# Kernel optimization log

Measured on AMD Instinct MI355X. Metric: run time of the kernel, lower is better.

Reference implementation:

```python
import jax, jax.numpy as jnp
import numpy as np

N, C, D_EMB = 4096, 8192, 512
SCALE = 3.0
KL_WEIGHT = 0.2


def _l2norm(x):
    # matches torch F.normalize(p=2, dim=-1) with eps clamp
    return x / jnp.maximum(jnp.linalg.norm(x, axis=-1, keepdims=True), 1e-12)


def setup_inputs() -> dict:
    key = jax.random.key(0)
    k1, k2, k3, k4 = jax.random.split(key, 4)
    X = jax.random.normal(k1, (N, D_EMB), dtype=jnp.float32)
    indices = jax.random.randint(k2, (N,), 0, N)
    T = jax.random.randint(k3, (N,), 0, C)
    proxies = jax.random.normal(k4, (C, D_EMB), dtype=jnp.float32) / 8.0
    sigmas_inv = jnp.full((C, D_EMB), np.log(np.e - 1.0), dtype=jnp.float32)
    return {"X": X, "indices": indices, "T": T, "proxies": proxies, "sigmas_inv": sigmas_inv}


def reference(X, indices, T, proxies, sigmas_inv):
    # per-class diagonal inverse-covariance weights s[c, d] = softplus(sigmas_inv)^2
    s = jax.nn.softplus(sigmas_inv) ** 2                        # (C, D)
    P = SCALE * _l2norm(proxies)                                # (C, D)
    Xn = SCALE * _l2norm(X)                                     # (N, D)
    # Mahalanobis-style distance D[n,c] = sum_d (x_nd - p_cd)^2 * s_cd
    Dmat = (Xn * Xn) @ s.T - 2.0 * (Xn @ (P * s).T) + jnp.sum(P * P * s, axis=-1)[None, :]  # (N, C)
    # log(softmax(-D)) == log_softmax(-D); one-hot targets (smoothing_const=0)
    logp = jax.nn.log_softmax(-Dmat, axis=-1)                   # (N, C)
    ce = -jnp.mean(logp[jnp.arange(Dmat.shape[0]), T])
    # KL regularizer: Sigma = 1/s, mu = normalized proxies
    Sig = 1.0 / s
    mus2 = _l2norm(proxies) ** 2
    kl = jnp.mean(jnp.sum(0.5 * (Sig + mus2 - 1.0 - jnp.log(Sig)), axis=-1))
    return ce + KL_WEIGHT * kl
```

## Files before the change

kernel.cpp:

```cpp
#include <hip/hip_runtime.h>
#include <hip/hip_bf16.h>
#include <cstdint>

#define N_ROWS 4096
#define N_CLS  8192
#define D_EMB  512
#define K_DIM  1024

using f32x4 = __attribute__((ext_vector_type(4))) float;

__device__ __forceinline__ float softplus_f(float v) {
  return (v > 20.f) ? v : log1pf(expf(v));
}

__device__ __forceinline__ unsigned short pack2_e4m3(float a, float b) {
  return (unsigned short)(__builtin_amdgcn_cvt_pk_fp8_f32(a, b, 0, false) & 0xffff);
}

__device__ __forceinline__ float e4m3_to_f(unsigned char v) {
  int e = (v >> 3) & 15, m = v & 7;
  float f;
  if (e) f = __uint_as_float((unsigned int)((e + 120) << 23) | ((unsigned int)m << 20));
  else   f = (float)m * 0.001953125f;
  return (v & 0x80) ? -f : f;
}

__device__ __forceinline__ float block_sum256(float v) {
  __shared__ float red[4];
  #pragma unroll
  for (int o = 32; o; o >>= 1) v += __shfl_xor(v, o);
  __syncthreads();
  if ((threadIdx.x & 63) == 0) red[threadIdx.x >> 6] = v;
  __syncthreads();
  return red[0] + red[1] + red[2] + red[3];
}

__device__ __forceinline__ void global_to_lds16(const void* g, void* l) {
  const __attribute__((address_space(1))) unsigned int* gp =
      reinterpret_cast<const __attribute__((address_space(1))) unsigned int*>(
          reinterpret_cast<uintptr_t>(g));
  __attribute__((address_space(3))) unsigned int* lp =
      reinterpret_cast<__attribute__((address_space(3))) unsigned int*>(
          reinterpret_cast<uintptr_t>(l));
  __builtin_amdgcn_global_load_lds(gp, lp, 16, 0, 0);
}

__global__ __launch_bounds__(256) void k_prep(const float* __restrict__ proxies,
                                              const float* __restrict__ sigmas_inv,
                                              const float* __restrict__ X,
                                              unsigned char* __restrict__ Bmat,
                                              unsigned char* __restrict__ Amat,
                                              float* __restrict__ tvec,
                                              float* __restrict__ klc) {
  const int bid = blockIdx.x;
  const int tid = threadIdx.x;
  if (bid < N_CLS) {
    const int c = bid;
    const float* p  = proxies    + (size_t)c * D_EMB;
    const float* si = sigmas_inv + (size_t)c * D_EMB;
    float2 p2 = ((const float2*)p)[tid];
    float ss = block_sum256(p2.x * p2.x + p2.y * p2.y);
    float invn = 1.0f / fmaxf(sqrtf(ss), 1e-12f);
    float2 s2 = ((const float2*)si)[tid];
    float sp0 = softplus_f(s2.x), sp1 = softplus_f(s2.y);
    float s0 = sp0 * sp0, s1 = sp1 * sp1;
    float pn0 = p2.x * invn, pn1 = p2.y * invn;
    float P0 = 3.0f * pn0, P1 = 3.0f * pn1;
    unsigned short* brow = (unsigned short*)(Bmat + (size_t)c * K_DIM);
    brow[tid]       = pack2_e4m3(s0, s1);
    brow[256 + tid] = pack2_e4m3(P0 * s0, P1 * s1);
    float tc = P0 * P0 * s0 + P1 * P1 * s1;
    float kl = 0.5f * (1.0f / s0 + pn0 * pn0 - 1.0f + 2.0f * logf(sp0))
             + 0.5f * (1.0f / s1 + pn1 * pn1 - 1.0f + 2.0f * logf(sp1));
    tc = block_sum256(tc);
    kl = block_sum256(kl);
    if (tid == 0) { tvec[c] = tc; klc[c] = kl; }
  } else {
    const int n = bid - N_CLS;
    const float* x = X + (size_t)n * D_EMB;
    float2 x2 = ((const float2*)x)[tid];
    float ss = block_sum256(x2.x * x2.x + x2.y * x2.y);
    float invn = 3.0f / fmaxf(sqrtf(ss), 1e-12f);
    float v0 = x2.x * invn, v1 = x2.y * invn;
    unsigned short* arow = (unsigned short*)(Amat + (size_t)n * K_DIM);
    arow[tid]       = pack2_e4m3(-v0 * v0, -v1 * v1);
    arow[256 + tid] = pack2_e4m3(2.0f * v0, 2.0f * v1);
  }
}

__global__ __launch_bounds__(256, 5) void k_gemm_lse(const unsigned char* __restrict__ Amat,
                                                     const unsigned char* __restrict__ Bmat,
                                                     const float* __restrict__ tvec,
                                                     float* __restrict__ Pm,
                                                     float* __restrict__ Psum) {
  __shared__ __align__(16) unsigned char lds[32768];
  const int tid  = threadIdx.x;
  const int lane = tid & 63;
  const int wave = tid >> 6;
  const int wr = wave >> 1, wc = wave & 1;
  const int swz  = ((int)blockIdx.x & 7) * 256 + ((int)blockIdx.x >> 3);
  const int rt   = swz & 31;
  const int ct   = swz >> 5;
  const int row0 = rt * 128;
  const int col0 = ct * 128;

  f32x4 acc[4][4];
  #pragma unroll
  for (int i = 0; i < 4; ++i)
    #pragma unroll
    for (int j = 0; j < 4; ++j) acc[i][j] = (f32x4){0.f, 0.f, 0.f, 0.f};

  const int arow = wr * 64 + (lane & 15);
  const int bcol = wc * 64 + (lane & 15);
  const int kb8  = (lane >> 4) * 8;

  const int f0  = tid * 16;
  const int f1  = 4096 + tid * 16;
  const int sf0 = f0 ^ (((f0 >> 7) & 7) << 4);
  const int sf1 = f1 ^ (((f1 >> 7) & 7) << 4);
  const unsigned char* gA0 = Amat + (size_t)(row0 + (sf0 >> 6)) * K_DIM + (sf0 & 63);
  const unsigned char* gA1 = Amat + (size_t)(row0 + (sf1 >> 6)) * K_DIM + (sf1 & 63);
  const unsigned char* gB0 = Bmat + (size_t)(col0 + (sf0 >> 6)) * K_DIM + (sf0 & 63);
  const unsigned char* gB1 = Bmat + (size_t)(col0 + (sf1 >> 6)) * K_DIM + (sf1 & 63);

  auto stg = [&](int slot, int ko) {
    unsigned char* la = lds + slot * 8192;
    unsigned char* lb = lds + 16384 + slot * 8192;
    global_to_lds16(gA0 + ko, la + f0);
    global_to_lds16(gA1 + ko, la + f1);
    global_to_lds16(gB0 + ko, lb + f0);
    global_to_lds16(gB1 + ko, lb + f1);
  };
  auto ld64 = [&](const unsigned char* base, int row, int kb) -> long {
    int f = row * 64 + kb;
    return *(const long*)(base + (f ^ (((f >> 7) & 7) << 4)));
  };

  stg(0, 0);
  __syncthreads();
  for (int t = 0; t < 16; ++t) {
    if (t < 15) stg((t + 1) & 1, (t + 1) * 64);
    const unsigned char* Ab = lds + (t & 1) * 8192;
    const unsigned char* Bb = lds + 16384 + (t & 1) * 8192;
    __builtin_amdgcn_s_setprio(1);
    #pragma unroll
    for (int ks = 0; ks < 64; ks += 32) {
      long a[4], b[4];
      #pragma unroll
      for (int mi = 0; mi < 4; ++mi) a[mi] = ld64(Ab, arow + mi * 16, ks + kb8);
      #pragma unroll
      for (int ni = 0; ni < 4; ++ni) b[ni] = ld64(Bb, bcol + ni * 16, ks + kb8);
      #pragma unroll
      for (int mi = 0; mi < 4; ++mi)
        #pragma unroll
        for (int ni = 0; ni < 4; ++ni)
          acc[mi][ni] = __builtin_amdgcn_mfma_f32_16x16x32_fp8_fp8(a[mi], b[ni], acc[mi][ni], 0, 0, 0);
    }
    __builtin_amdgcn_s_setprio(0);
    __syncthreads();
  }

  float (*ms)[2][2] = (float (*)[2][2])lds;
  float tc[4];
  #pragma unroll
  for (int ni = 0; ni < 4; ++ni)
    tc[ni] = tvec[col0 + wc * 64 + ni * 16 + (lane & 15)];

  #pragma unroll
  for (int mi = 0; mi < 4; ++mi) {
    #pragma unroll
    for (int j = 0; j < 4; ++j) {
      float z0 = acc[mi][0][j] - tc[0];
      float z1 = acc[mi][1][j] - tc[1];
      float z2 = acc[mi][2][j] - tc[2];
      float z3 = acc[mi][3][j] - tc[3];
      float m = fmaxf(fmaxf(z0, z1), fmaxf(z2, z3));
      #pragma unroll
      for (int o = 1; o < 16; o <<= 1) m = fmaxf(m, __shfl_xor(m, o));
      float s = __expf(z0 - m) + __expf(z1 - m) + __expf(z2 - m) + __expf(z3 - m);
      #pragma unroll
      for (int o = 1; o < 16; o <<= 1) s += __shfl_xor(s, o);
      if ((lane & 15) == 0) {
        int rloc = wr * 64 + mi * 16 + ((lane >> 4) << 2) + j;
        ms[rloc][wc][0] = m;
        ms[rloc][wc][1] = s;
      }
    }
  }
  __syncthreads();
  if (tid < 128) {
    float m0 = ms[tid][0][0], s0 = ms[tid][0][1];
    float m1 = ms[tid][1][0], s1 = ms[tid][1][1];
    float M = fmaxf(m0, m1);
    float S = s0 * __expf(m0 - M) + s1 * __expf(m1 - M);
    Pm  [(size_t)(row0 + tid) * 64 + ct] = M;
    Psum[(size_t)(row0 + tid) * 64 + ct] = S;
  }
}

__global__ __launch_bounds__(256) void k_red(const float* __restrict__ Pm,
                                             const float* __restrict__ Psum,
                                             const unsigned char* __restrict__ Amat,
                                             const unsigned char* __restrict__ Bmat,
                                             const float* __restrict__ tvec,
                                             const int* __restrict__ T,
                                             const float* __restrict__ klc,
                                             float* __restrict__ cep,
                                             float* __restrict__ klp) {
  __shared__ float tgt_s[16];
  const int b = blockIdx.x;
  const int tid = threadIdx.x;
  const int lane = tid & 63;
  const int w = tid >> 6;
  #pragma unroll
  for (int r = 0; r < 4; ++r) {
    const int loc = w * 4 + r;
    const int n = b * 16 + loc;
    const int c = T[n];
    uint4 av = *(const uint4*)(Amat + (size_t)n * K_DIM + lane * 16);
    uint4 bv = *(const uint4*)(Bmat + (size_t)c * K_DIM + lane * 16);
    const unsigned char* ab = (const unsigned char*)&av;
    const unsigned char* bb = (const unsigned char*)&bv;
    float s = 0.f;
    #pragma unroll
    for (int i = 0; i < 16; ++i) s += e4m3_to_f(ab[i]) * e4m3_to_f(bb[i]);
    #pragma unroll
    for (int o = 32; o; o >>= 1) s += __shfl_xor(s, o);
    if (lane == 0) tgt_s[loc] = s - tvec[c];
  }
  __syncthreads();
  const int loc = tid >> 4;
  const int n = b * 16 + loc;
  const int l4 = tid & 15;
  float4 pm = *(const float4*)(Pm   + (size_t)n * 64 + l4 * 4);
  float4 ps = *(const float4*)(Psum + (size_t)n * 64 + l4 * 4);
  float m = fmaxf(fmaxf(pm.x, pm.y), fmaxf(pm.z, pm.w));
  #pragma unroll
  for (int o = 1; o < 16; o <<= 1) m = fmaxf(m, __shfl_xor(m, o));
  float S = ps.x * __expf(pm.x - m) + ps.y * __expf(pm.y - m)
          + ps.z * __expf(pm.z - m) + ps.w * __expf(pm.w - m);
  #pragma unroll
  for (int o = 1; o < 16; o <<= 1) S += __shfl_xor(S, o);
  float ce = (l4 == 0) ? (m + logf(S) - tgt_s[loc]) : 0.f;
  float kl = (tid < 32) ? klc[b * 32 + tid] : 0.f;
  ce = block_sum256(ce);
  kl = block_sum256(kl);
  if (tid == 0) { cep[b] = ce; klp[b] = kl; }
}

__global__ __launch_bounds__(256) void k_fin2(const float* __restrict__ cep,
                                              const float* __restrict__ klp,
                                              float* __restrict__ out) {
  const int tid = threadIdx.x;
  float ce = block_sum256(cep[tid]);
  float kl = block_sum256(klp[tid]);
  if (tid == 0) out[0] = ce / (float)N_ROWS + 0.2f * (kl / (float)N_CLS);
}

extern "C" void kernel_launch(void* const* d_in, const int* in_sizes, int n_in,
                              void* d_out, int out_size, void* d_ws, size_t ws_size,
                              hipStream_t stream) {
  const float* X          = (const float*)d_in[0];
  const int*   T          = (const int*)d_in[2];
  const float* proxies    = (const float*)d_in[3];
  const float* sigmas_inv = (const float*)d_in[4];

  char* ws = (char*)d_ws;
  unsigned char* Amat = (unsigned char*)ws;
  unsigned char* Bmat = (unsigned char*)(ws + (4u << 20));
  float* tvec = (float*)(ws + (12u << 20));
  float* klc  = (float*)(ws + (12u << 20) + (32u << 10));
  float* Pm   = (float*)(ws + (12u << 20) + (64u << 10));
  float* Psum = (float*)(ws + (13u << 20) + (64u << 10));
  float* cep  = (float*)(ws + (14u << 20) + (64u << 10));
  float* klp  = (float*)(ws + (14u << 20) + (68u << 10));
  float* out  = (float*)d_out;

  hipLaunchKernelGGL(k_prep,     dim3(N_CLS + N_ROWS), dim3(256), 0, stream,
                     proxies, sigmas_inv, X, Bmat, Amat, tvec, klc);
  hipLaunchKernelGGL(k_gemm_lse, dim3(2048),           dim3(256), 0, stream,
                     Amat, Bmat, tvec, Pm, Psum);
  hipLaunchKernelGGL(k_red,      dim3(256),            dim3(256), 0, stream,
                     Pm, Psum, Amat, Bmat, tvec, T, klc, cep, klp);
  hipLaunchKernelGGL(k_fin2,     dim3(1),              dim3(256), 0, stream,
                     cep, klp, out);
}
```

Measured before the change: 106.0 us.

## Switch GEMM to 32x32x64 scaled FP8 MFMA with 256x128 tiles and 8 waves

Replaces the 16x16x32 FP8 MFMA inner loop with the MI355X 32x32x64 f8f6f4 scaled MFMA (unit scales), cutting the instruction count per k-step. Block tiles grow to 256x128 with 512 threads, and LDS is laid out so each lane reads one contiguous 32-byte fragment. The LSE epilogue is adapted to the 32x32 accumulator layout. The cost is more LDS per block and possibly lower occupancy. The row mapping in the epilogue must match the MFMA output layout for correctness.

```diff
diff --git a/kernel.cpp b/kernel.cpp
--- a/kernel.cpp
+++ b/kernel.cpp
@@ -7,7 +7,9 @@
 #define D_EMB  512
 #define K_DIM  1024
 
-using f32x4 = __attribute__((ext_vector_type(4))) float;
+using f32x4  = __attribute__((ext_vector_type(4)))  float;
+using f32x16 = __attribute__((ext_vector_type(16))) float;
+using i32x8  = __attribute__((ext_vector_type(8)))  int;
 
 __device__ __forceinline__ float softplus_f(float v) {
   return (v > 20.f) ? v : log1pf(expf(v));
@@ -88,107 +90,97 @@
   }
 }
 
-__global__ __launch_bounds__(256, 5) void k_gemm_lse(const unsigned char* __restrict__ Amat,
+__global__ __launch_bounds__(512, 4) void k_gemm_lse(const unsigned char* __restrict__ Amat,
                                                      const unsigned char* __restrict__ Bmat,
                                                      const float* __restrict__ tvec,
                                                      float* __restrict__ Pm,
                                                      float* __restrict__ Psum) {
-  __shared__ __align__(16) unsigned char lds[32768];
+  __shared__ __align__(16) unsigned char lds[49152];
   const int tid  = threadIdx.x;
   const int lane = tid & 63;
   const int wave = tid >> 6;
   const int wr = wave >> 1, wc = wave & 1;
-  const int swz  = ((int)blockIdx.x & 7) * 256 + ((int)blockIdx.x >> 3);
-  const int rt   = swz & 31;
-  const int ct   = swz >> 5;
-  const int row0 = rt * 128;
+  const int swz  = ((int)blockIdx.x & 7) * 128 + ((int)blockIdx.x >> 3);
+  const int rt   = swz & 15;
+  const int ct   = swz >> 4;
+  const int row0 = rt * 256;
   const int col0 = ct * 128;
 
-  f32x4 acc[4][4];
-  #pragma unroll
-  for (int i = 0; i < 4; ++i)
-    #pragma unroll
-    for (int j = 0; j < 4; ++j) acc[i][j] = (f32x4){0.f, 0.f, 0.f, 0.f};
-
-  const int arow = wr * 64 + (lane & 15);
-  const int bcol = wc * 64 + (lane & 15);
-  const int kb8  = (lane >> 4) * 8;
-
-  const int f0  = tid * 16;
-  const int f1  = 4096 + tid * 16;
-  const int sf0 = f0 ^ (((f0 >> 7) & 7) << 4);
-  const int sf1 = f1 ^ (((f1 >> 7) & 7) << 4);
-  const unsigned char* gA0 = Amat + (size_t)(row0 + (sf0 >> 6)) * K_DIM + (sf0 & 63);
-  const unsigned char* gA1 = Amat + (size_t)(row0 + (sf1 >> 6)) * K_DIM + (sf1 & 63);
-  const unsigned char* gB0 = Bmat + (size_t)(col0 + (sf0 >> 6)) * K_DIM + (sf0 & 63);
-  const unsigned char* gB1 = Bmat + (size_t)(col0 + (sf1 >> 6)) * K_DIM + (sf1 & 63);
+  const f32x16 Z = {0.f,0.f,0.f,0.f, 0.f,0.f,0.f,0.f, 0.f,0.f,0.f,0.f, 0.f,0.f,0.f,0.f};
+  f32x16 acc00 = Z, acc01 = Z, acc10 = Z, acc11 = Z;
+
+  const int gA0i = tid, gA1i = 512 + tid, gBi = tid;
+  auto srcA = [&](int g) {
+    int mi = g >> 7, l = (g & 127) >> 1, h = g & 1;
+    return Amat + (size_t)(row0 + mi * 32 + (l & 31)) * K_DIM + (l >> 5) * 32 + h * 16;
+  };
+  auto srcB = [&](int g) {
+    int nj = g >> 7, l = (g & 127) >> 1, h = g & 1;
+    return Bmat + (size_t)(col0 + nj * 32 + (l & 31)) * K_DIM + (l >> 5) * 32 + h * 16;
+  };
+  const unsigned char* gA0 = srcA(gA0i);
+  const unsigned char* gA1 = srcA(gA1i);
+  const unsigned char* gB0 = srcB(gBi);
 
   auto stg = [&](int slot, int ko) {
-    unsigned char* la = lds + slot * 8192;
-    unsigned char* lb = lds + 16384 + slot * 8192;
-    global_to_lds16(gA0 + ko, la + f0);
-    global_to_lds16(gA1 + ko, la + f1);
-    global_to_lds16(gB0 + ko, lb + f0);
-    global_to_lds16(gB1 + ko, lb + f1);
+    unsigned char* base = lds + slot * 24576;
+    global_to_lds16(gA0 + ko, base + gA0i * 16);
+    global_to_lds16(gA1 + ko, base + gA1i * 16);
+    global_to_lds16(gB0 + ko, base + 16384 + gBi * 16);
   };
-  auto ld64 = [&](const unsigned char* base, int row, int kb) -> long {
-    int f = row * 64 + kb;
-    return *(const long*)(base + (f ^ (((f >> 7) & 7) << 4)));
-  };
+
+  const int la32 = lane * 32;
+  const int offA0 = (wr * 2 + 0) * 2048 + la32;
+  const int offA1 = (wr * 2 + 1) * 2048 + la32;
+  const int offB0 = 16384 + (wc * 2 + 0) * 2048 + la32;
+  const int offB1 = 16384 + (wc * 2 + 1) * 2048 + la32;
 
   stg(0, 0);
   __syncthreads();
   for (int t = 0; t < 16; ++t) {
     if (t < 15) stg((t + 1) & 1, (t + 1) * 64);
-    const unsigned char* Ab = lds + (t & 1) * 8192;
-    const unsigned char* Bb = lds + 16384 + (t & 1) * 8192;
+    const unsigned char* S = lds + (t & 1) * 24576;
+    i32x8 a0 = *(const i32x8*)(S + offA0);
+    i32x8 a1 = *(const i32x8*)(S + offA1);
+    i32x8 b0 = *(const i32x8*)(S + offB0);
+    i32x8 b1 = *(const i32x8*)(S + offB1);
     __builtin_amdgcn_s_setprio(1);
-    #pragma unroll
-    for (int ks = 0; ks < 64; ks += 32) {
-      long a[4], b[4];
-      #pragma unroll
-      for (int mi = 0; mi < 4; ++mi) a[mi] = ld64(Ab, arow + mi * 16, ks + kb8);
-      #pragma unroll
-      for (int ni = 0; ni < 4; ++ni) b[ni] = ld64(Bb, bcol + ni * 16, ks + kb8);
-      #pragma unroll
-      for (int mi = 0; mi < 4; ++mi)
-        #pragma unroll
-        for (int ni = 0; ni < 4; ++ni)
-          acc[mi][ni] = __builtin_amdgcn_mfma_f32_16x16x32_fp8_fp8(a[mi], b[ni], acc[mi][ni], 0, 0, 0);
-    }
+    acc00 = __builtin_amdgcn_mfma_scale_f32_32x32x64_f8f6f4(a0, b0, acc00, 0, 0, 0, 0x7f7f7f7f, 0, 0x7f7f7f7f);
+    acc01 = __builtin_amdgcn_mfma_scale_f32_32x32x64_f8f6f4(a0, b1, acc01, 0, 0, 0, 0x7f7f7f7f, 0, 0x7f7f7f7f);
+    acc10 = __builtin_amdgcn_mfma_scale_f32_32x32x64_f8f6f4(a1, b0, acc10, 0, 0, 0, 0x7f7f7f7f, 0, 0x7f7f7f7f);
+    acc11 = __builtin_amdgcn_mfma_scale_f32_32x32x64_f8f6f4(a1, b1, acc11, 0, 0, 0, 0x7f7f7f7f, 0, 0x7f7f7f7f);
     __builtin_amdgcn_s_setprio(0);
     __syncthreads();
   }
 
   float (*ms)[2][2] = (float (*)[2][2])lds;
-  float tc[4];
-  #pragma unroll
-  for (int ni = 0; ni < 4; ++ni)
-    tc[ni] = tvec[col0 + wc * 64 + ni * 16 + (lane & 15)];
-
-  #pragma unroll
-  for (int mi = 0; mi < 4; ++mi) {
+  const float tc0 = tvec[col0 + wc * 64 + (lane & 31)];
+  const float tc1 = tvec[col0 + wc * 64 + 32 + (lane & 31)];
+  const int rbase = (lane >> 5) * 4;
+
+  #pragma unroll
+  for (int tm = 0; tm < 2; ++tm) {
+    const f32x16& CA = tm ? acc10 : acc00;
+    const f32x16& CB = tm ? acc11 : acc01;
     #pragma unroll
-    for (int j = 0; j < 4; ++j) {
-      float z0 = acc[mi][0][j] - tc[0];
-      float z1 = acc[mi][1][j] - tc[1];
-      float z2 = acc[mi][2][j] - tc[2];
-      float z3 = acc[mi][3][j] - tc[3];
-      float m = fmaxf(fmaxf(z0, z1), fmaxf(z2, z3));
+    for (int r = 0; r < 16; ++r) {
+      float z0 = CA[r] - tc0;
+      float z1 = CB[r] - tc1;
+      float m = fmaxf(z0, z1);
       #pragma unroll
-      for (int o = 1; o < 16; o <<= 1) m = fmaxf(m, __shfl_xor(m, o));
-      float s = __expf(z0 - m) + __expf(z1 - m) + __expf(z2 - m) + __expf(z3 - m);
+      for (int o = 1; o < 32; o <<= 1) m = fmaxf(m, __shfl_xor(m, o));
+      float s = __expf(z0 - m) + __expf(z1 - m);
       #pragma unroll
-      for (int o = 1; o < 16; o <<= 1) s += __shfl_xor(s, o);
-      if ((lane & 15) == 0) {
-        int rloc = wr * 64 + mi * 16 + ((lane >> 4) << 2) + j;
+      for (int o = 1; o < 32; o <<= 1) s += __shfl_xor(s, o);
+      if ((lane & 31) == 0) {
+        int rloc = wr * 64 + tm * 32 + (r & 3) + 8 * (r >> 2) + rbase;
         ms[rloc][wc][0] = m;
         ms[rloc][wc][1] = s;
       }
     }
   }
   __syncthreads();
-  if (tid < 128) {
+  if (tid < 256) {
     float m0 = ms[tid][0][0], s0 = ms[tid][0][1];
     float m1 = ms[tid][1][0], s1 = ms[tid][1][1];
     float M = fmaxf(m0, m1);
@@ -278,7 +270,7 @@
 
   hipLaunchKernelGGL(k_prep,     dim3(N_CLS + N_ROWS), dim3(256), 0, stream,
                      proxies, sigmas_inv, X, Bmat, Amat, tvec, klc);
-  hipLaunchKernelGGL(k_gemm_lse, dim3(2048),           dim3(256), 0, stream,
+  hipLaunchKernelGGL(k_gemm_lse, dim3(1024),           dim3(512), 0, stream,
                      Amat, Bmat, tvec, Pm, Psum);
   hipLaunchKernelGGL(k_red,      dim3(256),            dim3(256), 0, stream,
                      Pm, Psum, Amat, Bmat, tvec, T, klc, cep, klp);
```

New measurement: 382.1 us. +260.4%, slower.

## Enlarge GEMM tiles to 256x256 with 512-thread blocks and precomputed LDS offsets

Applied to the files above, without the earlier changes.

The fused GEMM+logsumexp kernel now uses 256x256 output tiles with 8 waves per block, each wave owning a 128x64 sub-tile. That gives 8x4 MFMA accumulators per wave and more operand reuse per LDS load. Swizzled LDS offsets are precomputed once outside the k-loop. The partial-LSE layout shrinks to 32 column tiles per row, so the reduction and final kernels are resized to match. The larger tiles raise register pressure and LDS use to 64KB per block, and with only 512 blocks occupancy and wave balance across CUs drop.

```diff
diff --git a/kernel.cpp b/kernel.cpp
--- a/kernel.cpp
+++ b/kernel.cpp
@@ -88,70 +88,72 @@
   }
 }
 
-__global__ __launch_bounds__(256, 5) void k_gemm_lse(const unsigned char* __restrict__ Amat,
+__global__ __launch_bounds__(512, 2) void k_gemm_lse(const unsigned char* __restrict__ Amat,
                                                      const unsigned char* __restrict__ Bmat,
                                                      const float* __restrict__ tvec,
                                                      float* __restrict__ Pm,
                                                      float* __restrict__ Psum) {
-  __shared__ __align__(16) unsigned char lds[32768];
+  __shared__ __align__(16) unsigned char lds[65536];
   const int tid  = threadIdx.x;
   const int lane = tid & 63;
   const int wave = tid >> 6;
-  const int wr = wave >> 1, wc = wave & 1;
-  const int swz  = ((int)blockIdx.x & 7) * 256 + ((int)blockIdx.x >> 3);
-  const int rt   = swz & 31;
-  const int ct   = swz >> 5;
-  const int row0 = rt * 128;
-  const int col0 = ct * 128;
-
-  f32x4 acc[4][4];
-  #pragma unroll
-  for (int i = 0; i < 4; ++i)
+  const int wr = wave >> 2, wc = wave & 3;
+  const int swz  = ((int)blockIdx.x & 7) * 64 + ((int)blockIdx.x >> 3);
+  const int rt   = swz & 15;
+  const int ct   = swz >> 4;
+  const int row0 = rt * 256;
+  const int col0 = ct * 256;
+
+  f32x4 acc[8][4];
+  #pragma unroll
+  for (int i = 0; i < 8; ++i)
     #pragma unroll
     for (int j = 0; j < 4; ++j) acc[i][j] = (f32x4){0.f, 0.f, 0.f, 0.f};
 
-  const int arow = wr * 64 + (lane & 15);
-  const int bcol = wc * 64 + (lane & 15);
-  const int kb8  = (lane >> 4) * 8;
-
   const int f0  = tid * 16;
-  const int f1  = 4096 + tid * 16;
   const int sf0 = f0 ^ (((f0 >> 7) & 7) << 4);
-  const int sf1 = f1 ^ (((f1 >> 7) & 7) << 4);
   const unsigned char* gA0 = Amat + (size_t)(row0 + (sf0 >> 6)) * K_DIM + (sf0 & 63);
-  const unsigned char* gA1 = Amat + (size_t)(row0 + (sf1 >> 6)) * K_DIM + (sf1 & 63);
   const unsigned char* gB0 = Bmat + (size_t)(col0 + (sf0 >> 6)) * K_DIM + (sf0 & 63);
-  const unsigned char* gB1 = Bmat + (size_t)(col0 + (sf1 >> 6)) * K_DIM + (sf1 & 63);
 
   auto stg = [&](int slot, int ko) {
-    unsigned char* la = lds + slot * 8192;
-    unsigned char* lb = lds + 16384 + slot * 8192;
-    global_to_lds16(gA0 + ko, la + f0);
-    global_to_lds16(gA1 + ko, la + f1);
-    global_to_lds16(gB0 + ko, lb + f0);
-    global_to_lds16(gB1 + ko, lb + f1);
+    unsigned char* la = lds + slot * 16384;
+    unsigned char* lb = lds + 32768 + slot * 16384;
+    global_to_lds16(gA0 + ko,          la + f0);
+    global_to_lds16(gA0 + 131072 + ko, la + 8192 + f0);
+    global_to_lds16(gB0 + ko,          lb + f0);
+    global_to_lds16(gB0 + 131072 + ko, lb + 8192 + f0);
   };
-  auto ld64 = [&](const unsigned char* base, int row, int kb) -> long {
-    int f = row * 64 + kb;
-    return *(const long*)(base + (f ^ (((f >> 7) & 7) << 4)));
-  };
+
+  auto swzf = [](int f) { return f ^ (((f >> 7) & 7) << 4); };
+  const int l15 = lane & 15;
+  const int kb8 = (lane >> 4) * 8;
+  int offA[8][2], offB[4][2];
+  #pragma unroll
+  for (int mi = 0; mi < 8; ++mi)
+    #pragma unroll
+    for (int s = 0; s < 2; ++s)
+      offA[mi][s] = swzf((wr * 128 + mi * 16 + l15) * 64 + s * 32 + kb8);
+  #pragma unroll
+  for (int ni = 0; ni < 4; ++ni)
+    #pragma unroll
+    for (int s = 0; s < 2; ++s)
+      offB[ni][s] = 32768 + swzf((wc * 64 + ni * 16 + l15) * 64 + s * 32 + kb8);
 
   stg(0, 0);
   __syncthreads();
   for (int t = 0; t < 16; ++t) {
     if (t < 15) stg((t + 1) & 1, (t + 1) * 64);
-    const unsigned char* Ab = lds + (t & 1) * 8192;
-    const unsigned char* Bb = lds + 16384 + (t & 1) * 8192;
+    const unsigned char* S = lds + (t & 1) * 16384;
     __builtin_amdgcn_s_setprio(1);
     #pragma unroll
-    for (int ks = 0; ks < 64; ks += 32) {
-      long a[4], b[4];
-      #pragma unroll
-      for (int mi = 0; mi < 4; ++mi) a[mi] = ld64(Ab, arow + mi * 16, ks + kb8);
-      #pragma unroll
-      for (int ni = 0; ni < 4; ++ni) b[ni] = ld64(Bb, bcol + ni * 16, ks + kb8);
-      #pragma unroll
-      for (int mi = 0; mi < 4; ++mi)
+    for (int s = 0; s < 2; ++s) {
+      long a[8], b[4];
+      #pragma unroll
+      for (int mi = 0; mi < 8; ++mi) a[mi] = *(const long*)(S + offA[mi][s]);
+      #pragma unroll
+      for (int ni = 0; ni < 4; ++ni) b[ni] = *(const long*)(S + offB[ni][s]);
+      #pragma unroll
+      for (int mi = 0; mi < 8; ++mi)
         #pragma unroll
         for (int ni = 0; ni < 4; ++ni)
           acc[mi][ni] = __builtin_amdgcn_mfma_f32_16x16x32_fp8_fp8(a[mi], b[ni], acc[mi][ni], 0, 0, 0);
@@ -160,14 +162,14 @@
     __syncthreads();
   }
 
-  float (*ms)[2][2] = (float (*)[2][2])lds;
+  float (*ms)[4][2] = (float (*)[4][2])lds;
   float tc[4];
   #pragma unroll
   for (int ni = 0; ni < 4; ++ni)
-    tc[ni] = tvec[col0 + wc * 64 + ni * 16 + (lane & 15)];
-
-  #pragma unroll
-  for (int mi = 0; mi < 4; ++mi) {
+    tc[ni] = tvec[col0 + wc * 64 + ni * 16 + l15];
+
+  #pragma unroll
+  for (int mi = 0; mi < 8; ++mi) {
     #pragma unroll
     for (int j = 0; j < 4; ++j) {
       float z0 = acc[mi][0][j] - tc[0];
@@ -180,21 +182,24 @@
       float s = __expf(z0 - m) + __expf(z1 - m) + __expf(z2 - m) + __expf(z3 - m);
       #pragma unroll
       for (int o = 1; o < 16; o <<= 1) s += __shfl_xor(s, o);
-      if ((lane & 15) == 0) {
-        int rloc = wr * 64 + mi * 16 + ((lane >> 4) << 2) + j;
+      if (l15 == 0) {
+        int rloc = wr * 128 + mi * 16 + ((lane >> 4) << 2) + j;
         ms[rloc][wc][0] = m;
         ms[rloc][wc][1] = s;
       }
     }
   }
   __syncthreads();
-  if (tid < 128) {
+  if (tid < 256) {
     float m0 = ms[tid][0][0], s0 = ms[tid][0][1];
     float m1 = ms[tid][1][0], s1 = ms[tid][1][1];
-    float M = fmaxf(m0, m1);
-    float S = s0 * __expf(m0 - M) + s1 * __expf(m1 - M);
-    Pm  [(size_t)(row0 + tid) * 64 + ct] = M;
-    Psum[(size_t)(row0 + tid) * 64 + ct] = S;
+    float m2 = ms[tid][2][0], s2 = ms[tid][2][1];
+    float m3 = ms[tid][3][0], s3 = ms[tid][3][1];
+    float M = fmaxf(fmaxf(m0, m1), fmaxf(m2, m3));
+    float S = s0 * __expf(m0 - M) + s1 * __expf(m1 - M)
+            + s2 * __expf(m2 - M) + s3 * __expf(m3 - M);
+    Pm  [(size_t)(row0 + tid) * 32 + ct] = M;
+    Psum[(size_t)(row0 + tid) * 32 + ct] = S;
   }
 }
 
@@ -207,15 +212,15 @@
                                              const float* __restrict__ klc,
                                              float* __restrict__ cep,
                                              float* __restrict__ klp) {
-  __shared__ float tgt_s[16];
+  __shared__ float tgt_s[32];
   const int b = blockIdx.x;
   const int tid = threadIdx.x;
   const int lane = tid & 63;
   const int w = tid >> 6;
   #pragma unroll
-  for (int r = 0; r < 4; ++r) {
-    const int loc = w * 4 + r;
-    const int n = b * 16 + loc;
+  for (int r = 0; r < 8; ++r) {
+    const int loc = w * 8 + r;
+    const int n = b * 32 + loc;
     const int c = T[n];
     uint4 av = *(const uint4*)(Amat + (size_t)n * K_DIM + lane * 16);
     uint4 bv = *(const uint4*)(Bmat + (size_t)c * K_DIM + lane * 16);
@@ -229,20 +234,20 @@
     if (lane == 0) tgt_s[loc] = s - tvec[c];
   }
   __syncthreads();
-  const int loc = tid >> 4;
-  const int n = b * 16 + loc;
-  const int l4 = tid & 15;
-  float4 pm = *(const float4*)(Pm   + (size_t)n * 64 + l4 * 4);
-  float4 ps = *(const float4*)(Psum + (size_t)n * 64 + l4 * 4);
+  const int loc = tid >> 3;
+  const int n = b * 32 + loc;
+  const int l8 = tid & 7;
+  float4 pm = *(const float4*)(Pm   + (size_t)n * 32 + l8 * 4);
+  float4 ps = *(const float4*)(Psum + (size_t)n * 32 + l8 * 4);
   float m = fmaxf(fmaxf(pm.x, pm.y), fmaxf(pm.z, pm.w));
   #pragma unroll
-  for (int o = 1; o < 16; o <<= 1) m = fmaxf(m, __shfl_xor(m, o));
+  for (int o = 1; o < 8; o <<= 1) m = fmaxf(m, __shfl_xor(m, o));
   float S = ps.x * __expf(pm.x - m) + ps.y * __expf(pm.y - m)
           + ps.z * __expf(pm.z - m) + ps.w * __expf(pm.w - m);
   #pragma unroll
-  for (int o = 1; o < 16; o <<= 1) S += __shfl_xor(S, o);
-  float ce = (l4 == 0) ? (m + logf(S) - tgt_s[loc]) : 0.f;
-  float kl = (tid < 32) ? klc[b * 32 + tid] : 0.f;
+  for (int o = 1; o < 8; o <<= 1) S += __shfl_xor(S, o);
+  float ce = (l8 == 0) ? (m + logf(S) - tgt_s[loc]) : 0.f;
+  float kl = (tid < 64) ? klc[b * 64 + tid] : 0.f;
   ce = block_sum256(ce);
   kl = block_sum256(kl);
   if (tid == 0) { cep[b] = ce; klp[b] = kl; }
@@ -252,8 +257,8 @@
                                               const float* __restrict__ klp,
                                               float* __restrict__ out) {
   const int tid = threadIdx.x;
-  float ce = block_sum256(cep[tid]);
-  float kl = block_sum256(klp[tid]);
+  float ce = block_sum256(tid < 128 ? cep[tid] : 0.f);
+  float kl = block_sum256(tid < 128 ? klp[tid] : 0.f);
   if (tid == 0) out[0] = ce / (float)N_ROWS + 0.2f * (kl / (float)N_CLS);
 }
 
@@ -271,16 +276,16 @@
   float* tvec = (float*)(ws + (12u << 20));
   float* klc  = (float*)(ws + (12u << 20) + (32u << 10));
   float* Pm   = (float*)(ws + (12u << 20) + (64u << 10));
-  float* Psum = (float*)(ws + (13u << 20) + (64u << 10));
-  float* cep  = (float*)(ws + (14u << 20) + (64u << 10));
-  float* klp  = (float*)(ws + (14u << 20) + (68u << 10));
+  float* Psum = (float*)(ws + (12u << 20) + (576u << 10));
+  float* cep  = (float*)(ws + (12u << 20) + (1088u << 10));
+  float* klp  = (float*)(ws + (12u << 20) + (1092u << 10));
   float* out  = (float*)d_out;
 
   hipLaunchKernelGGL(k_prep,     dim3(N_CLS + N_ROWS), dim3(256), 0, stream,
                      proxies, sigmas_inv, X, Bmat, Amat, tvec, klc);
-  hipLaunchKernelGGL(k_gemm_lse, dim3(2048),           dim3(256), 0, stream,
+  hipLaunchKernelGGL(k_gemm_lse, dim3(512),            dim3(512), 0, stream,
                      Amat, Bmat, tvec, Pm, Psum);
-  hipLaunchKernelGGL(k_red,      dim3(256),            dim3(256), 0, stream,
+  hipLaunchKernelGGL(k_red,      dim3(128),            dim3(256), 0, stream,
                      Pm, Psum, Amat, Bmat, tvec, T, klc, cep, klp);
   hipLaunchKernelGGL(k_fin2,     dim3(1),              dim3(256), 0, stream,
                      cep, klp, out);
```

Measured after the change: 112.3 us. +5.9%, slower.

## Use 256x128 GEMM tiles with 8 waves and fuse target logit extraction into epilogue

Applied to the files above, without the earlier changes.

The GEMM+logsumexp kernel now uses 512-thread blocks covering 256 rows by 128 columns, so each B tile staged into LDS is reused by twice as many rows and the grid halves to 1024 blocks. The epilogue also writes the target-class logit directly from the accumulators when a thread holds column T[row]. This removes the separate fp8 dot-product recomputation in the reduction kernel. It costs more LDS per block (48KB) and a per-element compare against T in the epilogue, and occupancy per CU may drop.

```diff
diff --git a/kernel.cpp b/kernel.cpp
--- a/kernel.cpp
+++ b/kernel.cpp
@@ -15,14 +15,6 @@
 
 __device__ __forceinline__ unsigned short pack2_e4m3(float a, float b) {
   return (unsigned short)(__builtin_amdgcn_cvt_pk_fp8_f32(a, b, 0, false) & 0xffff);
-}
-
-__device__ __forceinline__ float e4m3_to_f(unsigned char v) {
-  int e = (v >> 3) & 15, m = v & 7;
-  float f;
-  if (e) f = __uint_as_float((unsigned int)((e + 120) << 23) | ((unsigned int)m << 20));
-  else   f = (float)m * 0.001953125f;
-  return (v & 0x80) ? -f : f;
 }
 
 __device__ __forceinline__ float block_sum256(float v) {
@@ -88,20 +80,26 @@
   }
 }
 
-__global__ __launch_bounds__(256, 5) void k_gemm_lse(const unsigned char* __restrict__ Amat,
+__global__ __launch_bounds__(512, 4) void k_gemm_lse(const unsigned char* __restrict__ Amat,
                                                      const unsigned char* __restrict__ Bmat,
                                                      const float* __restrict__ tvec,
+                                                     const int* __restrict__ T,
                                                      float* __restrict__ Pm,
-                                                     float* __restrict__ Psum) {
-  __shared__ __align__(16) unsigned char lds[32768];
+                                                     float* __restrict__ Psum,
+                                                     float* __restrict__ tgt) {
+  union SMem {
+    struct { unsigned char As[2][16384]; unsigned char Bs[2][8192]; } st;
+    float ms[256][2][2];
+  };
+  __shared__ SMem sm;
   const int tid  = threadIdx.x;
   const int lane = tid & 63;
   const int wave = tid >> 6;
   const int wr = wave >> 1, wc = wave & 1;
-  const int swz  = ((int)blockIdx.x & 7) * 256 + ((int)blockIdx.x >> 3);
-  const int rt   = swz & 31;
-  const int ct   = swz >> 5;
-  const int row0 = rt * 128;
+  const int swz  = ((int)blockIdx.x & 7) * 128 + ((int)blockIdx.x >> 3);
+  const int rt   = swz & 15;
+  const int ct   = swz >> 4;
+  const int row0 = rt * 256;
   const int col0 = ct * 128;
 
   f32x4 acc[4][4];
@@ -114,34 +112,32 @@
   const int bcol = wc * 64 + (lane & 15);
   const int kb8  = (lane >> 4) * 8;
 
-  const int f0  = tid * 16;
-  const int f1  = 4096 + tid * 16;
-  const int sf0 = f0 ^ (((f0 >> 7) & 7) << 4);
-  const int sf1 = f1 ^ (((f1 >> 7) & 7) << 4);
-  const unsigned char* gA0 = Amat + (size_t)(row0 + (sf0 >> 6)) * K_DIM + (sf0 & 63);
-  const unsigned char* gA1 = Amat + (size_t)(row0 + (sf1 >> 6)) * K_DIM + (sf1 & 63);
-  const unsigned char* gB0 = Bmat + (size_t)(col0 + (sf0 >> 6)) * K_DIM + (sf0 & 63);
-  const unsigned char* gB1 = Bmat + (size_t)(col0 + (sf1 >> 6)) * K_DIM + (sf1 & 63);
-
-  auto stg = [&](int slot, int ko) {
-    unsigned char* la = lds + slot * 8192;
-    unsigned char* lb = lds + 16384 + slot * 8192;
-    global_to_lds16(gA0 + ko, la + f0);
-    global_to_lds16(gA1 + ko, la + f1);
-    global_to_lds16(gB0 + ko, lb + f0);
-    global_to_lds16(gB1 + ko, lb + f1);
+  auto stage = [&](int buf, int ko) {
+    #pragma unroll
+    for (int rep = 0; rep < 2; ++rep) {
+      int f  = rep * 8192 + tid * 16;
+      int sf = f ^ (((f >> 7) & 7) << 4);
+      global_to_lds16(Amat + (size_t)(row0 + (sf >> 6)) * K_DIM + ko + (sf & 63),
+                      &sm.st.As[buf][f]);
+    }
+    {
+      int f  = tid * 16;
+      int sf = f ^ (((f >> 7) & 7) << 4);
+      global_to_lds16(Bmat + (size_t)(col0 + (sf >> 6)) * K_DIM + ko + (sf & 63),
+                      &sm.st.Bs[buf][f]);
+    }
   };
   auto ld64 = [&](const unsigned char* base, int row, int kb) -> long {
     int f = row * 64 + kb;
     return *(const long*)(base + (f ^ (((f >> 7) & 7) << 4)));
   };
 
-  stg(0, 0);
+  stage(0, 0);
   __syncthreads();
   for (int t = 0; t < 16; ++t) {
-    if (t < 15) stg((t + 1) & 1, (t + 1) * 64);
-    const unsigned char* Ab = lds + (t & 1) * 8192;
-    const unsigned char* Bb = lds + 16384 + (t & 1) * 8192;
+    if (t < 15) stage((t + 1) & 1, (t + 1) * 64);
+    const unsigned char* Ab = sm.st.As[t & 1];
+    const unsigned char* Bb = sm.st.Bs[t & 1];
     __builtin_amdgcn_s_setprio(1);
     #pragma unroll
     for (int ks = 0; ks < 64; ks += 32) {
@@ -160,37 +156,44 @@
     __syncthreads();
   }
 
-  float (*ms)[2][2] = (float (*)[2][2])lds;
+  const int l15 = lane & 15;
   float tc[4];
   #pragma unroll
   for (int ni = 0; ni < 4; ++ni)
-    tc[ni] = tvec[col0 + wc * 64 + ni * 16 + (lane & 15)];
+    tc[ni] = tvec[col0 + wc * 64 + ni * 16 + l15];
+  const int cbase = col0 + wc * 64 + l15;
 
   #pragma unroll
   for (int mi = 0; mi < 4; ++mi) {
     #pragma unroll
     for (int j = 0; j < 4; ++j) {
+      const int grow = row0 + wr * 64 + mi * 16 + ((lane >> 4) << 2) + j;
+      const int d = T[grow] - cbase;
       float z0 = acc[mi][0][j] - tc[0];
       float z1 = acc[mi][1][j] - tc[1];
       float z2 = acc[mi][2][j] - tc[2];
       float z3 = acc[mi][3][j] - tc[3];
+      if (d == 0)  tgt[grow] = z0;
+      if (d == 16) tgt[grow] = z1;
+      if (d == 32) tgt[grow] = z2;
+      if (d == 48) tgt[grow] = z3;
       float m = fmaxf(fmaxf(z0, z1), fmaxf(z2, z3));
       #pragma unroll
       for (int o = 1; o < 16; o <<= 1) m = fmaxf(m, __shfl_xor(m, o));
       float s = __expf(z0 - m) + __expf(z1 - m) + __expf(z2 - m) + __expf(z3 - m);
       #pragma unroll
       for (int o = 1; o < 16; o <<= 1) s += __shfl_xor(s, o);
-      if ((lane & 15) == 0) {
+      if (l15 == 0) {
         int rloc = wr * 64 + mi * 16 + ((lane >> 4) << 2) + j;
-        ms[rloc][wc][0] = m;
-        ms[rloc][wc][1] = s;
+        sm.ms[rloc][wc][0] = m;
+        sm.ms[rloc][wc][1] = s;
       }
     }
   }
   __syncthreads();
-  if (tid < 128) {
-    float m0 = ms[tid][0][0], s0 = ms[tid][0][1];
-    float m1 = ms[tid][1][0], s1 = ms[tid][1][1];
+  if (tid < 256) {
+    float m0 = sm.ms[tid][0][0], s0 = sm.ms[tid][0][1];
+    float m1 = sm.ms[tid][1][0], s1 = sm.ms[tid][1][1];
     float M = fmaxf(m0, m1);
     float S = s0 * __expf(m0 - M) + s1 * __expf(m1 - M);
     Pm  [(size_t)(row0 + tid) * 64 + ct] = M;
@@ -200,37 +203,13 @@
 
 __global__ __launch_bounds__(256) void k_red(const float* __restrict__ Pm,
                                              const float* __restrict__ Psum,
-                                             const unsigned char* __restrict__ Amat,
-                                             const unsigned char* __restrict__ Bmat,
-                                             const float* __restrict__ tvec,
-                                             const int* __restrict__ T,
+                                             const float* __restrict__ tgt,
                                              const float* __restrict__ klc,
                                              float* __restrict__ cep,
                                              float* __restrict__ klp) {
-  __shared__ float tgt_s[16];
   const int b = blockIdx.x;
   const int tid = threadIdx.x;
-  const int lane = tid & 63;
-  const int w = tid >> 6;
-  #pragma unroll
-  for (int r = 0; r < 4; ++r) {
-    const int loc = w * 4 + r;
-    const int n = b * 16 + loc;
-    const int c = T[n];
-    uint4 av = *(const uint4*)(Amat + (size_t)n * K_DIM + lane * 16);
-    uint4 bv = *(const uint4*)(Bmat + (size_t)c * K_DIM + lane * 16);
-    const unsigned char* ab = (const unsigned char*)&av;
-    const unsigned char* bb = (const unsigned char*)&bv;
-    float s = 0.f;
-    #pragma unroll
-    for (int i = 0; i < 16; ++i) s += e4m3_to_f(ab[i]) * e4m3_to_f(bb[i]);
-    #pragma unroll
-    for (int o = 32; o; o >>= 1) s += __shfl_xor(s, o);
-    if (lane == 0) tgt_s[loc] = s - tvec[c];
-  }
-  __syncthreads();
-  const int loc = tid >> 4;
-  const int n = b * 16 + loc;
+  const int n = b * 16 + (tid >> 4);
   const int l4 = tid & 15;
   float4 pm = *(const float4*)(Pm   + (size_t)n * 64 + l4 * 4);
   float4 ps = *(const float4*)(Psum + (size_t)n * 64 + l4 * 4);
@@ -241,7 +220,7 @@
           + ps.z * __expf(pm.z - m) + ps.w * __expf(pm.w - m);
   #pragma unroll
   for (int o = 1; o < 16; o <<= 1) S += __shfl_xor(S, o);
-  float ce = (l4 == 0) ? (m + logf(S) - tgt_s[loc]) : 0.f;
+  float ce = (l4 == 0) ? (m + logf(S) - tgt[n]) : 0.f;
   float kl = (tid < 32) ? klc[b * 32 + tid] : 0.f;
   ce = block_sum256(ce);
   kl = block_sum256(kl);
@@ -272,16 +251,17 @@
   float* klc  = (float*)(ws + (12u << 20) + (32u << 10));
   float* Pm   = (float*)(ws + (12u << 20) + (64u << 10));
   float* Psum = (float*)(ws + (13u << 20) + (64u << 10));
-  float* cep  = (float*)(ws + (14u << 20) + (64u << 10));
-  float* klp  = (float*)(ws + (14u << 20) + (68u << 10));
+  float* tgt  = (float*)(ws + (14u << 20) + (64u << 10));
+  float* cep  = (float*)(ws + (14u << 20) + (80u << 10));
+  float* klp  = (float*)(ws + (14u << 20) + (84u << 10));
   float* out  = (float*)d_out;
 
   hipLaunchKernelGGL(k_prep,     dim3(N_CLS + N_ROWS), dim3(256), 0, stream,
                      proxies, sigmas_inv, X, Bmat, Amat, tvec, klc);
-  hipLaunchKernelGGL(k_gemm_lse, dim3(2048),           dim3(256), 0, stream,
-                     Amat, Bmat, tvec, Pm, Psum);
+  hipLaunchKernelGGL(k_gemm_lse, dim3(1024),           dim3(512), 0, stream,
+                     Amat, Bmat, tvec, T, Pm, Psum, tgt);
   hipLaunchKernelGGL(k_red,      dim3(256),            dim3(256), 0, stream,
-                     Pm, Psum, Amat, Bmat, tvec, T, klc, cep, klp);
+                     Pm, Psum, tgt, klc, cep, klp);
   hipLaunchKernelGGL(k_fin2,     dim3(1),              dim3(256), 0, stream,
                      cep, klp, out);
 }
```

Measured after the change: 88.90 us, median of 2. -16.1%, faster.
